# Kernel tuning notes

Measured on AMD Instinct MI355X. Metric: run time of the kernel, lower is better.

## Reference

```python
import jax, jax.numpy as jnp
import numpy as np

N, D, NUM_CLASSES = 4096, 1024, 1000


def setup_inputs() -> dict:
    key = jax.random.key(0)
    k1, k2 = jax.random.split(key)
    output = jax.random.normal(k1, (N, D), dtype=jnp.float32)
    target = jax.random.randint(k2, (N,), 0, NUM_CLASSES, dtype=jnp.int64)
    return {"output": output, "target": target}


def reference(output, target):
    # k1: strictly-lower-triangular part of the gram matrix [N, N]
    gram = output @ output.T
    k1 = jnp.tril(gram, -1)
    # k2: strictly-lower-triangular label-equality mask (vectorized form of
    # the original O(N^2) python double loop)
    eq = (target[:, None] == target[None, :]).astype(output.dtype)
    k2 = jnp.tril(eq, -1)
    return -(jnp.sum(k1 * k2) / (jnp.sum(k2) * jnp.linalg.norm(k1)))
```

## Files before the change

kernel.cpp:

```cpp
#include <hip/hip_runtime.h>
#include <hip/hip_bf16.h>


typedef __attribute__((ext_vector_type(8))) short short8;
typedef __attribute__((ext_vector_type(4))) float f32x4;

#define N_ROWS 4096
#define D_DIM  1024
#define N_CLS  1000
#define NTIL   136
#define NK     32

__device__ __forceinline__ unsigned short f2bf(float f) {
  unsigned u = __float_as_uint(f);
  u += 0x7fffu + ((u >> 16) & 1u);
  return (unsigned short)(u >> 16);
}

__device__ __forceinline__ void gload16(const short* g, const char* l) {
  __builtin_amdgcn_global_load_lds(
      (const __attribute__((address_space(1))) unsigned*)g,
      (__attribute__((address_space(3))) unsigned*)(void*)l, 16, 0, 0);
}

__global__ void __launch_bounds__(256) kconv(const float* __restrict__ A,
                                             short* __restrict__ Ab,
                                             double* __restrict__ rowp) {
  __shared__ double wr2[4];
  const int tid = threadIdx.x, lane = tid & 63, w = tid >> 6;
  const int row0 = blockIdx.x * 8;
  double ls = 0.0;
#pragma unroll
  for (int rr = 0; rr < 2; ++rr) {
    const int i = row0 + w * 2 + rr;
    const float4* src = (const float4*)(A + (size_t)i * D_DIM);
    short4* dst = (short4*)(Ab + (size_t)i * D_DIM);
    float s = 0.f;
#pragma unroll
    for (int c = 0; c < 4; ++c) {
      const float4 v = src[lane + c * 64];
      s += v.x * v.x + v.y * v.y + v.z * v.z + v.w * v.w;
      short4 o;
      o.x = (short)f2bf(v.x); o.y = (short)f2bf(v.y);
      o.z = (short)f2bf(v.z); o.w = (short)f2bf(v.w);
      dst[lane + c * 64] = o;
    }
#pragma unroll
    for (int off = 32; off; off >>= 1) s += __shfl_down(s, off);
    if (lane == 0) ls += (double)s;
  }
  if (lane == 0) wr2[w] = ls;
  __syncthreads();
  if (tid == 0) rowp[blockIdx.x] = wr2[0] + wr2[1] + wr2[2] + wr2[3];
}

__global__ void __launch_bounds__(512, 2) kmain(const float* __restrict__ A,
                                                const int* __restrict__ target,
                                                const short* __restrict__ Ab,
                                                double* __restrict__ frobp,
                                                double* __restrict__ cssp,
                                                int* __restrict__ cntp) {
  __shared__ __align__(16) char smem[65600];
  const int tid = threadIdx.x, lane = tid & 63, w = tid >> 6;

  if (blockIdx.x < NTIL) {
    double* wredd = (double*)(smem + 65536);

    const int b = (blockIdx.x & 7) * 17 + (blockIdx.x >> 3);
    int bi = (int)((sqrtf(8.f * (float)b + 1.f) - 1.f) * 0.5f);
    while ((bi + 1) * (bi + 2) / 2 <= b) ++bi;
    while (bi * (bi + 1) / 2 > b) --bi;
    const int bj = b - bi * (bi + 1) / 2;
    const bool diag = (bi == bj);

    const short* Pa = Ab + (size_t)(bi * 256) * D_DIM;
    const short* Pb = Ab + (size_t)(bj * 256) * D_DIM;

    f32x4 acc[8][4];
#pragma unroll
    for (int m = 0; m < 8; ++m)
#pragma unroll
      for (int n = 0; n < 4; ++n) acc[m][n] = (f32x4){0.f, 0.f, 0.f, 0.f};

    const int wr = w >> 2, wc = w & 3;
    const int row16 = lane & 15, ck = lane >> 4;

    const int sr = tid >> 2;
    const int scS = (tid & 3) ^ ((sr >> 1) & 3);
    const size_t g0 = (size_t)sr * D_DIM + scS * 8;
    const size_t g1 = (size_t)(sr + 128) * D_DIM + scS * 8;
    const int l0 = w * 1024;
    const int l1 = 8192 + w * 1024;

#define ASB(buf) (smem + (buf) * 16384)
#define BSB(buf) (smem + 32768 + (buf) * 16384)

#define STAGE(buf, k0)                                                      \
    do {                                                                    \
      gload16(Pa + g0 + (k0), ASB(buf) + l0);                               \
      gload16(Pa + g1 + (k0), ASB(buf) + l1);                               \
      gload16(Pb + g0 + (k0), BSB(buf) + l0);                               \
      gload16(Pb + g1 + (k0), BSB(buf) + l1);                               \
    } while (0)

#define SWZ(R) (((R) * 32) + ((ck ^ (((R) >> 1) & 3)) * 8))

#define COMPUTE(buf)                                                        \
    do {                                                                    \
      short8 af[8], bf[4];                                                  \
      _Pragma("unroll")                                                     \
      for (int m = 0; m < 8; ++m)                                           \
        af[m] = *(const short8*)((short*)ASB(buf) + SWZ(wr * 128 + m * 16 + row16)); \
      _Pragma("unroll")                                                     \
      for (int n = 0; n < 4; ++n)                                           \
        bf[n] = *(const short8*)((short*)BSB(buf) + SWZ(wc * 64 + n * 16 + row16)); \
      _Pragma("unroll")                                                     \
      for (int m = 0; m < 8; ++m)                                           \
        _Pragma("unroll")                                                   \
        for (int n = 0; n < 4; ++n)                                         \
          acc[m][n] = __builtin_amdgcn_mfma_f32_16x16x32_bf16(af[m], bf[n], \
                                                              acc[m][n], 0, 0, 0); \
    } while (0)

    STAGE(0, 0);
    int cur = 0;
#pragma unroll 1
    for (int t = 0; t < NK - 1; ++t) {
      STAGE(cur ^ 1, (t + 1) * 32);
      asm volatile("s_waitcnt vmcnt(4)" ::: "memory");
      __builtin_amdgcn_sched_barrier(0);
      __builtin_amdgcn_s_barrier();
      __builtin_amdgcn_sched_barrier(0);
      COMPUTE(cur);
      asm volatile("s_waitcnt lgkmcnt(0)" ::: "memory");
      __builtin_amdgcn_sched_barrier(0);
      __builtin_amdgcn_s_barrier();
      __builtin_amdgcn_sched_barrier(0);
      cur ^= 1;
    }
    asm volatile("s_waitcnt vmcnt(0)" ::: "memory");
    __builtin_amdgcn_sched_barrier(0);
    __builtin_amdgcn_s_barrier();
    __builtin_amdgcn_sched_barrier(0);
    COMPUTE(cur);
#undef STAGE
#undef COMPUTE
#undef SWZ
#undef ASB
#undef BSB

    float fs = 0.f;
    if (!diag) {
#pragma unroll
      for (int m = 0; m < 8; ++m)
#pragma unroll
        for (int n = 0; n < 4; ++n)
#pragma unroll
          for (int q = 0; q < 4; ++q) fs += acc[m][n][q] * acc[m][n][q];
    } else {
      const int rbase = (lane >> 4) * 4, cbase = lane & 15;
#pragma unroll
      for (int m = 0; m < 8; ++m)
#pragma unroll
        for (int n = 0; n < 4; ++n)
#pragma unroll
          for (int q = 0; q < 4; ++q) {
            const int rl = wr * 128 + m * 16 + rbase + q;
            const int cl = wc * 64 + n * 16 + cbase;
            if (rl > cl) fs += acc[m][n][q] * acc[m][n][q];
          }
    }
#pragma unroll
    for (int off = 32; off; off >>= 1) fs += __shfl_down(fs, off);
    if (lane == 0) wredd[w] = (double)fs;
    __syncthreads();
    if (tid == 0) {
      double t = 0.0;
#pragma unroll
      for (int i = 0; i < 8; ++i) t += wredd[i];
      frobp[b] = t;
    }
  } else {
    int* list = (int*)smem;
    int* lcnt = (int*)(smem + 16384);
    float* wredf = (float*)(smem + 16400);
    const int c = blockIdx.x - NTIL;
    if (c >= N_CLS) return;
    if (tid == 0) *lcnt = 0;
    __syncthreads();
    for (int j = tid; j < N_ROWS; j += 512)
      if (target[j] == c) { int p = atomicAdd(lcnt, 1); list[p] = j; }
    __syncthreads();
    const int n = *lcnt;
    float2 acc = make_float2(0.f, 0.f);
    for (int m = 0; m < n; ++m) {
      const float2 v = *(const float2*)(A + (size_t)list[m] * D_DIM + tid * 2);
      acc.x += v.x; acc.y += v.y;
    }
    float s = acc.x * acc.x + acc.y * acc.y;
#pragma unroll
    for (int off = 32; off; off >>= 1) s += __shfl_down(s, off);
    if (lane == 0) wredf[w] = s;
    __syncthreads();
    if (tid == 0) {
      float t = 0.f;
#pragma unroll
      for (int i = 0; i < 8; ++i) t += wredf[i];
      cssp[c] = (double)t;
      cntp[c] = n;
    }
  }
}

__global__ void __launch_bounds__(256) kfinal(const double* __restrict__ rowp,
                                              const double* __restrict__ cssp,
                                              const int* __restrict__ cntp,
                                              const double* __restrict__ frobp,
                                              float* __restrict__ out) {
  __shared__ double red[256];
  const int tid = threadIdx.x;
  double lsum = rowp[tid] + rowp[tid + 256];
  double lcss = 0.0, lcnn = 0.0, lfr = 0.0;
  for (int c = tid; c < N_CLS; c += 256) {
    lcss += cssp[c];
    const double nc = (double)cntp[c];
    lcnn += nc * nc;
  }
  if (tid < NTIL) lfr = frobp[tid];

  double vals[4] = {lsum, lcss, lcnn, lfr};
  double res[4];
  for (int v = 0; v < 4; ++v) {
    red[tid] = vals[v];
    __syncthreads();
    for (int s = 128; s; s >>= 1) {
      if (tid < s) red[tid] += red[tid + s];
      __syncthreads();
    }
    res[v] = red[0];
    __syncthreads();
  }
  if (tid == 0) {
    const double sumr = res[0], css = res[1], cnn = res[2], frob = res[3];
    const double S1 = 0.5 * (css - sumr);
    const double S2 = 0.5 * (cnn - (double)N_ROWS);
    const double S3 = frob;
    out[0] = (float)(-(S1 / (S2 * sqrt(S3))));
  }
}

extern "C" void kernel_launch(void* const* d_in, const int* in_sizes, int n_in,
                              void* d_out, int out_size, void* d_ws, size_t ws_size,
                              hipStream_t stream) {
  const float* A = (const float*)d_in[0];
  const int* target = (const int*)d_in[1];
  float* out = (float*)d_out;

  char* ws = (char*)d_ws;
  short*  Ab    = (short*)ws;
  double* rowp  = (double*)(ws + 8388608);
  double* cssp  = (double*)(ws + 8388608 + 4096);
  int*    cntp  = (int*)   (ws + 8388608 + 4096 + 8000);
  double* frobp = (double*)(ws + 8388608 + 4096 + 8000 + 4096);

  kconv<<<512, 256, 0, stream>>>(A, Ab, rowp);
  kmain<<<NTIL + N_CLS, 512, 0, stream>>>(A, target, Ab, frobp, cssp, cntp);
  kfinal<<<1, 256, 0, stream>>>(rowp, cssp, cntp, frobp, out);
}
```

Before: 46.95 us.

## Rework Gram GEMM mainloop into K64 double-buffered phased MFMA schedule

```diff
diff --git a/kernel.cpp b/kernel.cpp
--- a/kernel.cpp
+++ b/kernel.cpp
@@ -9,7 +9,6 @@
 #define D_DIM  1024
 #define N_CLS  1000
 #define NTIL   136
-#define NK     32
 
 __device__ __forceinline__ unsigned short f2bf(float f) {
   unsigned u = __float_as_uint(f);
@@ -60,12 +59,10 @@
                                                 double* __restrict__ frobp,
                                                 double* __restrict__ cssp,
                                                 int* __restrict__ cntp) {
-  __shared__ __align__(16) char smem[65600];
+  __shared__ __align__(16) char smem[131072];
   const int tid = threadIdx.x, lane = tid & 63, w = tid >> 6;
 
   if (blockIdx.x < NTIL) {
-    double* wredd = (double*)(smem + 65536);
-
     const int b = (blockIdx.x & 7) * 17 + (blockIdx.x >> 3);
     int bi = (int)((sqrtf(8.f * (float)b + 1.f) - 1.f) * 0.5f);
     while ((bi + 1) * (bi + 2) / 2 <= b) ++bi;
@@ -76,78 +73,107 @@
     const short* Pa = Ab + (size_t)(bi * 256) * D_DIM;
     const short* Pb = Ab + (size_t)(bj * 256) * D_DIM;
 
+    short* As0 = (short*)smem;
+    short* As1 = (short*)(smem + 32768);
+    short* Bs0 = (short*)(smem + 65536);
+    short* Bs1 = (short*)(smem + 98304);
+
     f32x4 acc[8][4];
 #pragma unroll
     for (int m = 0; m < 8; ++m)
 #pragma unroll
       for (int n = 0; n < 4; ++n) acc[m][n] = (f32x4){0.f, 0.f, 0.f, 0.f};
 
-    const int wr = w >> 2, wc = w & 3;
+    const int wm = w >> 2, wn = w & 3;
     const int row16 = lane & 15, ck = lane >> 4;
 
     const int sr = tid >> 2;
     const int scS = (tid & 3) ^ ((sr >> 1) & 3);
-    const size_t g0 = (size_t)sr * D_DIM + scS * 8;
-    const size_t g1 = (size_t)(sr + 128) * D_DIM + scS * 8;
-    const int l0 = w * 1024;
-    const int l1 = 8192 + w * 1024;
-
-#define ASB(buf) (smem + (buf) * 16384)
-#define BSB(buf) (smem + 32768 + (buf) * 16384)
-
-#define STAGE(buf, k0)                                                      \
+
+#define STAGEU(P, BUF, h, kt)                                               \
     do {                                                                    \
-      gload16(Pa + g0 + (k0), ASB(buf) + l0);                               \
-      gload16(Pa + g1 + (k0), ASB(buf) + l1);                               \
-      gload16(Pb + g0 + (k0), BSB(buf) + l0);                               \
-      gload16(Pb + g1 + (k0), BSB(buf) + l1);                               \
+      const short* _g = (P) + ((size_t)((h) * 128 + sr)) * D_DIM + (kt) * 64 + scS * 8; \
+      gload16(_g,      (const char*)(BUF) + (h) * 8192 + w * 1024);         \
+      gload16(_g + 32, (const char*)(BUF) + 16384 + (h) * 8192 + w * 1024); \
     } while (0)
 
-#define SWZ(R) (((R) * 32) + ((ck ^ (((R) >> 1) & 3)) * 8))
-
-#define COMPUTE(buf)                                                        \
-    do {                                                                    \
-      short8 af[8], bf[4];                                                  \
-      _Pragma("unroll")                                                     \
-      for (int m = 0; m < 8; ++m)                                           \
-        af[m] = *(const short8*)((short*)ASB(buf) + SWZ(wr * 128 + m * 16 + row16)); \
-      _Pragma("unroll")                                                     \
-      for (int n = 0; n < 4; ++n)                                           \
-        bf[n] = *(const short8*)((short*)BSB(buf) + SWZ(wc * 64 + n * 16 + row16)); \
-      _Pragma("unroll")                                                     \
-      for (int m = 0; m < 8; ++m)                                           \
-        _Pragma("unroll")                                                   \
-        for (int n = 0; n < 4; ++n)                                         \
-          acc[m][n] = __builtin_amdgcn_mfma_f32_16x16x32_bf16(af[m], bf[n], \
-                                                              acc[m][n], 0, 0, 0); \
-    } while (0)
-
-    STAGE(0, 0);
-    int cur = 0;
+#define RD_A(BUF, MH)                                                       \
+    _Pragma("unroll") for (int ks = 0; ks < 2; ++ks)                        \
+    _Pragma("unroll") for (int m = 0; m < 4; ++m) {                         \
+      const int R = wm * 128 + ((MH) * 4 + m) * 16 + row16;                 \
+      a[ks][m] = *(const short8*)((const char*)(BUF) + ks * 16384 + R * 64  \
+                                  + ((ck ^ ((R >> 1) & 3)) << 4));          \
+    }
+#define RD_B(DST, BUF, NH)                                                  \
+    _Pragma("unroll") for (int ks = 0; ks < 2; ++ks)                        \
+    _Pragma("unroll") for (int n = 0; n < 2; ++n) {                         \
+      const int R = wn * 64 + ((NH) * 2 + n) * 16 + row16;                  \
+      DST[ks][n] = *(const short8*)((const char*)(BUF) + ks * 16384 + R * 64\
+                                    + ((ck ^ ((R >> 1) & 3)) << 4));        \
+    }
+#define PH_MFMA(MO, NO, BB)                                                 \
+    __builtin_amdgcn_s_setprio(1);                                          \
+    _Pragma("unroll") for (int ks = 0; ks < 2; ++ks)                        \
+    _Pragma("unroll") for (int m = 0; m < 4; ++m)                           \
+    _Pragma("unroll") for (int n = 0; n < 2; ++n)                           \
+      acc[(MO) + m][(NO) + n] = __builtin_amdgcn_mfma_f32_16x16x32_bf16(    \
+          a[ks][m], BB[ks][n], acc[(MO) + m][(NO) + n], 0, 0, 0);           \
+    __builtin_amdgcn_s_setprio(0);
+#define BAR __builtin_amdgcn_s_barrier()
+#define VM0 asm volatile("s_waitcnt vmcnt(0)" ::: "memory")
+
+    STAGEU(Pa, As0, 0, 0); STAGEU(Pa, As0, 1, 0);
+    STAGEU(Pb, Bs0, 0, 0); STAGEU(Pb, Bs0, 1, 0);
+    VM0;
+    BAR;
+
 #pragma unroll 1
-    for (int t = 0; t < NK - 1; ++t) {
-      STAGE(cur ^ 1, (t + 1) * 32);
-      asm volatile("s_waitcnt vmcnt(4)" ::: "memory");
-      __builtin_amdgcn_sched_barrier(0);
-      __builtin_amdgcn_s_barrier();
-      __builtin_amdgcn_sched_barrier(0);
-      COMPUTE(cur);
-      asm volatile("s_waitcnt lgkmcnt(0)" ::: "memory");
-      __builtin_amdgcn_sched_barrier(0);
-      __builtin_amdgcn_s_barrier();
-      __builtin_amdgcn_sched_barrier(0);
-      cur ^= 1;
-    }
-    asm volatile("s_waitcnt vmcnt(0)" ::: "memory");
-    __builtin_amdgcn_sched_barrier(0);
-    __builtin_amdgcn_s_barrier();
-    __builtin_amdgcn_sched_barrier(0);
-    COMPUTE(cur);
-#undef STAGE
-#undef COMPUTE
-#undef SWZ
-#undef ASB
-#undef BSB
+    for (int it = 0; it < 8; ++it) {
+      const int t1 = 2 * it + 1, t2 = 2 * it + 2;
+      short8 a[2][4], bq0[2][2], b[2][2];
+      RD_A(As0, 0); RD_B(bq0, Bs0, 0);
+      STAGEU(Pa, As1, 0, t1); STAGEU(Pa, As1, 1, t1);
+      BAR;
+      PH_MFMA(0, 0, bq0);
+      BAR;
+      RD_B(b, Bs0, 1);
+      STAGEU(Pb, Bs1, 0, t1); STAGEU(Pb, Bs1, 1, t1);
+      BAR;
+      PH_MFMA(0, 2, b);
+      BAR;
+      RD_A(As0, 1);
+      BAR;
+      PH_MFMA(4, 2, b);
+      BAR;
+      PH_MFMA(4, 0, bq0);
+      BAR;
+      VM0;
+      BAR;
+      RD_A(As1, 0); RD_B(bq0, Bs1, 0);
+      if (it < 7) { STAGEU(Pa, As0, 0, t2); STAGEU(Pa, As0, 1, t2); }
+      BAR;
+      PH_MFMA(0, 0, bq0);
+      BAR;
+      RD_B(b, Bs1, 1);
+      if (it < 7) { STAGEU(Pb, Bs0, 0, t2); STAGEU(Pb, Bs0, 1, t2); }
+      BAR;
+      PH_MFMA(0, 2, b);
+      BAR;
+      RD_A(As1, 1);
+      BAR;
+      PH_MFMA(4, 2, b);
+      BAR;
+      PH_MFMA(4, 0, bq0);
+      BAR;
+      VM0;
+      BAR;
+    }
+#undef STAGEU
+#undef RD_A
+#undef RD_B
+#undef PH_MFMA
+#undef BAR
+#undef VM0
 
     float fs = 0.f;
     if (!diag) {
@@ -165,13 +191,14 @@
         for (int n = 0; n < 4; ++n)
 #pragma unroll
           for (int q = 0; q < 4; ++q) {
-            const int rl = wr * 128 + m * 16 + rbase + q;
-            const int cl = wc * 64 + n * 16 + cbase;
+            const int rl = wm * 128 + m * 16 + rbase + q;
+            const int cl = wn * 64 + n * 16 + cbase;
             if (rl > cl) fs += acc[m][n][q] * acc[m][n][q];
           }
     }
 #pragma unroll
     for (int off = 32; off; off >>= 1) fs += __shfl_down(fs, off);
+    double* wredd = (double*)smem;
     if (lane == 0) wredd[w] = (double)fs;
     __syncthreads();
     if (tid == 0) {
```

Result: faster. 45.51 us (median of 2 runs) (-3.1%).
